# Kernel optimization log

Hardware: AMD Instinct MI355X
Metric: run time of the kernel (lower is better)

Reference implementation:

```python
import jax, jax.numpy as jnp
import numpy as np

MEAN_DEG = 3.8
QS = (2, 4, 8, 16, 32, 64)
POOL_DIM = 100
BP_ITERS = 10


def _bn(x, g, b):
    # BatchNorm1d in training mode: biased batch statistics over the node dim
    m = x.mean(0)
    v = ((x - m) ** 2).mean(0)
    return g * (x - m) * jax.lax.rsqrt(v + 1e-5) + b


def _gcn_sparse(x, src, dst, n, w, b):
    # GCNConv: add self loops, symmetric deg^-1/2 normalization, scatter-add aggregation
    loop = jnp.arange(n, dtype=src.dtype)
    s2 = jnp.concatenate([src, loop])
    d2 = jnp.concatenate([dst, loop])
    deg = jax.ops.segment_sum(jnp.ones(s2.shape[0], x.dtype), d2, num_segments=n)
    dinv = jnp.where(deg > 0, jax.lax.rsqrt(deg), 0.0)
    norm = (dinv[s2] * dinv[d2])[:, None]
    return jax.ops.segment_sum((x @ w)[s2] * norm, d2, num_segments=n) + b


def _gcn_dense(x, adj, w, b):
    # GCN on the dense pooled adjacency (pooled graphs are fully connected)
    n = adj.shape[-1]
    A = adj + jnp.eye(n, dtype=adj.dtype)
    d = A.sum(-1)
    dinv = jnp.where(d > 0, jax.lax.rsqrt(d), 0.0)
    An = dinv[:, :, None] * A * dinv[:, None, :]
    return jnp.einsum('bij,bjd->bid', An, x @ w) + b


def _bp(src, dst, n, q, beta, seed):
    # SBM-style belief propagation: iterate node marginals psi [n,q] for a fixed
    # number of sweeps; coupling exp(beta), global external field ~ mean_degree.
    key = jax.random.fold_in(jax.random.key(42), seed)
    psi0 = jax.nn.softmax(jax.random.normal(key, (n, q), jnp.float32), -1)
    eb = jnp.expm1(beta)

    def step(psi, _):
        msg = jax.ops.segment_sum(jnp.log1p(eb * psi[src]), dst, num_segments=n)
        field = (MEAN_DEG * beta / n) * psi.sum(0)
        return jax.nn.softmax(msg - field, -1), None

    psi, _ = jax.lax.scan(step, psi0, None, length=BP_ITERS)
    return psi


def _forward(x, w11, b11, g11, be11, w12, b12, g12, be12, w13, b13, g13, be13,
             bp_betas, pool_w, pool_b,
             w21, b21, g21, be21, w22, b22, g22, be22, w23, b23, g23, be23,
             fc1_w, fc1_b, fc2_w, fc2_b, edge_index, num_graphs):
    n = x.shape[0]
    B = num_graphs
    N = n // B
    src, dst = edge_index[0], edge_index[1]
    # per-graph dense adjacency (edge_index_to_csr -> todense, duplicates sum)
    adj = jnp.zeros((B, N, N), x.dtype).at[src // N, src % N, dst % N].add(1.0)

    # stage 1: three GCN + BN layers on the raw graph
    x11 = _bn(_gcn_sparse(x, src, dst, n, w11, b11), g11, be11)
    x12 = _bn(_gcn_sparse(x11, src, dst, n, w12, b12), g12, be12)
    x13 = _bn(_gcn_sparse(x12, src, dst, n, w13, b13), g13, be13)
    x1_out = jnp.concatenate([x11, x12, x13], -1).reshape(B, N, -1).max(1)  # [B,90]

    # six belief-propagation runs -> concat assignments [n, 2+4+...+64 = 126]
    s1 = jnp.concatenate([_bp(src, dst, n, q, bp_betas[i], i) for i, q in enumerate(QS)], -1)
    s1 = s1 @ pool_w + pool_b  # [n, 100]

    # dense diff-pool
    s1 = jax.nn.softmax(s1.reshape(B, N, POOL_DIM), -1)
    p1_x = jnp.einsum('bnk,bnd->bkd', s1, x13.reshape(B, N, -1))   # [B,100,30]
    p1_adj = jnp.einsum('bnk,bnm,bml->bkl', s1, adj, s1)           # [B,100,100]

    # stage 2: three dense GCN + BN layers on pooled graphs
    C = 30
    x21 = _bn(_gcn_dense(p1_x, p1_adj, w21, b21).reshape(-1, C), g21, be21)
    x22 = _bn(_gcn_dense(x21.reshape(B, POOL_DIM, C), p1_adj, w22, b22).reshape(-1, C), g22, be22)
    x23 = _bn(_gcn_dense(x22.reshape(B, POOL_DIM, C), p1_adj, w23, b23).reshape(-1, C), g23, be23)
    x2_out = jnp.concatenate([x21, x22, x23], -1).reshape(B, POOL_DIM, -1).max(1)  # [B,90]

    conv_out = jnp.concatenate([x1_out, x2_out], -1)  # [B,180]
    out = jax.nn.relu(conv_out @ fc1_w + fc1_b) @ fc2_w + fc2_b  # dropout p=0 -> identity
    return out, jnp.zeros((1,), x.dtype)


def setup_inputs() -> dict:
    key = jax.random.key(0)
    B, N, EP = 64, 1024, 8192
    ks = jax.random.split(key, 24)
    x = jax.random.normal(ks[0], (B * N, 3), jnp.float32)
    off = (jnp.arange(B, dtype=jnp.int32) * N)[:, None]
    src = (jax.random.randint(ks[1], (B, EP), 0, N, jnp.int32) + off).reshape(-1)
    dst = (jax.random.randint(ks[2], (B, EP), 0, N, jnp.int32) + off).reshape(-1)
    edge_index = jnp.stack([src, dst])

    def lin(k, i, o):
        return jax.random.normal(k, (i, o), jnp.float32) / np.sqrt(i)

    p = {}
    dims1 = [(3, 30), (30, 30), (30, 30)]
    for idx, (i, o) in enumerate(dims1, 1):
        p['w1%d' % idx] = lin(ks[2 + idx], i, o)
        p['b1%d' % idx] = jnp.zeros((o,), jnp.float32)
        p['g1%d' % idx] = jnp.ones((o,), jnp.float32)
        p['be1%d' % idx] = jnp.zeros((o,), jnp.float32)
    for idx in (1, 2, 3):
        p['w2%d' % idx] = lin(ks[8 + idx], 30, 30)
        p['b2%d' % idx] = jnp.zeros((30,), jnp.float32)
        p['g2%d' % idx] = jnp.ones((30,), jnp.float32)
        p['be2%d' % idx] = jnp.zeros((30,), jnp.float32)
    qs = np.array(QS, np.float32)
    p['bp_betas'] = jnp.asarray(np.log(qs / (np.sqrt(MEAN_DEG) - 1.0) + 1.0))
    p['pool_w'] = lin(ks[15], 126, 100); p['pool_b'] = jnp.zeros((100,), jnp.float32)
    p['fc1_w'] = lin(ks[16], 180, 50); p['fc1_b'] = jnp.zeros((50,), jnp.float32)
    p['fc2_w'] = lin(ks[17], 50, 6); p['fc2_b'] = jnp.zeros((6,), jnp.float32)
    return {'x': x, 'edge_index': edge_index, 'num_graphs': B, **p}


def reference(x, edge_index, num_graphs, w11, b11, g11, be11, w12, b12, g12, be12,
              w13, b13, g13, be13, bp_betas, pool_w, pool_b,
              w21, b21, g21, be21, w22, b22, g22, be22, w23, b23, g23, be23,
              fc1_w, fc1_b, fc2_w, fc2_b):
    return _forward(x, w11, b11, g11, be11, w12, b12, g12, be12, w13, b13, g13, be13,
                    bp_betas, pool_w, pool_b,
                    w21, b21, g21, be21, w22, b22, g22, be22, w23, b23, g23, be23,
                    fc1_w, fc1_b, fc2_w, fc2_b, edge_index, num_graphs)
```

## Files before the change

### kernel.cpp

```cpp
#include <hip/hip_runtime.h>
#include <stdint.h>
#include <float.h>


constexpr int NN    = 65536;
constexpr int NEDGE = 524288;
constexpr int NBG   = 64;

__constant__ int cQS[6]   = {2,4,8,16,32,64};

__device__ __forceinline__ void tf2x32(uint32_t k0, uint32_t k1, uint32_t x0, uint32_t x1,
                                       uint32_t& o0, uint32_t& o1){
  uint32_t ks[3] = {k0, k1, k0 ^ k1 ^ 0x1BD11BDAu};
  x0 += ks[0]; x1 += ks[1];
  const int RA[4] = {13,15,26,6}, RB[4] = {17,29,16,24};
  #pragma unroll
  for (int i=0;i<5;i++){
    const int* r = (i&1)? RB : RA;
    #pragma unroll
    for (int j=0;j<4;j++){
      x0 += x1;
      x1 = (x1 << r[j]) | (x1 >> (32 - r[j]));
      x1 ^= x0;
    }
    x0 += ks[(i+1)%3];
    x1 += ks[(i+2)%3] + (uint32_t)(i+1);
  }
  o0 = x0; o1 = x1;
}

__device__ __forceinline__ float erfinv32(float xx){
  #pragma clang fp contract(off)
  float w = -log1pf(-xx*xx);
  float p;
  if (w < 5.0f){
    w = w - 2.5f;
    p = 2.81022636e-08f;
    p = 3.43273939e-07f  + p*w;
    p = -3.5233877e-06f  + p*w;
    p = -4.39150654e-06f + p*w;
    p = 0.00021858087f   + p*w;
    p = -0.00125372503f  + p*w;
    p = -0.00417768164f  + p*w;
    p = 0.246640727f     + p*w;
    p = 1.50140941f      + p*w;
  } else {
    w = sqrtf(w) - 3.0f;
    p = -0.000200214257f;
    p = 0.000100950558f  + p*w;
    p = 0.00134934322f   + p*w;
    p = -0.00367342844f  + p*w;
    p = 0.00573950773f   + p*w;
    p = -0.0076224613f   + p*w;
    p = 0.00943887047f   + p*w;
    p = 1.00167406f      + p*w;
    p = 2.83297682f      + p*w;
  }
  return p*xx;
}

__global__ __launch_bounds__(256) void k_count(const int* __restrict__ src, const int* __restrict__ dst,
                                               int* __restrict__ degi, int* __restrict__ dego){
  int e = blockIdx.x*256 + threadIdx.x;
  if (e >= NEDGE) return;
  atomicAdd(&degi[dst[e]], 1);
  atomicAdd(&dego[src[e]], 1);
}

__global__ __launch_bounds__(256) void k_scan1(const int* __restrict__ deg, int* __restrict__ rp,
                                               int* __restrict__ bsum){
  __shared__ int lds[256];
  int b = blockIdx.x, t = threadIdx.x;
  lds[t] = deg[b*256 + t];
  __syncthreads();
  for (int s=1;s<256;s<<=1){
    int add = (t>=s)? lds[t-s] : 0;
    __syncthreads();
    lds[t] += add;
    __syncthreads();
  }
  rp[b*256 + t + 1] = lds[t];
  if (t==0 && b==0) rp[0] = 0;
  if (t==255) bsum[b] = lds[255];
}

__global__ __launch_bounds__(256) void k_scan2(int* __restrict__ bsum){
  __shared__ int lds[256];
  int t = threadIdx.x;
  lds[t] = bsum[t];
  __syncthreads();
  for (int s=1;s<256;s<<=1){
    int add = (t>=s)? lds[t-s] : 0;
    __syncthreads();
    lds[t] += add;
    __syncthreads();
  }
  bsum[t] = (t==0)? 0 : lds[t-1];
}

__global__ __launch_bounds__(256) void k_scan3(int* __restrict__ rp, const int* __restrict__ bsum){
  int b = blockIdx.x, t = threadIdx.x;
  rp[b*256 + t + 1] += bsum[b];
}

__global__ __launch_bounds__(256) void k_fill(const int* __restrict__ key, const int* __restrict__ rp,
                                              int* __restrict__ cnt, int* __restrict__ colbuf){
  int e = blockIdx.x*256 + threadIdx.x;
  if (e >= NEDGE) return;
  int d = key[e];
  int p = atomicAdd(&cnt[d], 1);
  colbuf[rp[d] + p] = e;
}

__global__ __launch_bounds__(256) void k_sortrow(const int* __restrict__ rp, int* __restrict__ colbuf,
                                                 const int* __restrict__ other){
  int v = blockIdx.x*256 + threadIdx.x;
  if (v >= NN) return;
  int s0 = rp[v], s1 = rp[v+1];
  for (int i=s0+1;i<s1;i++){
    int key = colbuf[i]; int j = i-1;
    while (j>=s0 && colbuf[j]>key){ colbuf[j+1]=colbuf[j]; j--; }
    colbuf[j+1] = key;
  }
  for (int i=s0;i<s1;i++) colbuf[i] = other[colbuf[i]];
}

__global__ __launch_bounds__(256) void k_dinv(const int* __restrict__ degi, float* __restrict__ dinv){
  int v = blockIdx.x*256 + threadIdx.x;
  if (v >= NN) return;
  dinv[v] = 1.0f / sqrtf((float)(degi[v] + 1));
}

template<int CIN>
__global__ __launch_bounds__(256) void k_mm30(const float* __restrict__ x, const float* __restrict__ w,
                                              float* __restrict__ h, int nrow){
  __shared__ float ws[CIN*30];
  int t = threadIdx.x;
  for (int i=t;i<CIN*30;i+=256) ws[i] = w[i];
  __syncthreads();
  int id = blockIdx.x*256 + t;
  if (id >= nrow*30) return;
  int v = id/30, j = id - v*30;
  const float* xr = x + v*CIN;
  float acc = 0.f;
  #pragma unroll
  for (int k=0;k<CIN;k++) acc += xr[k]*ws[k*30+j];
  h[id] = acc;
}

__global__ __launch_bounds__(256) void k_gcn_agg(const float* __restrict__ h, const int* __restrict__ rp,
    const int* __restrict__ col, const float* __restrict__ dinv, const float* __restrict__ bias,
    float* __restrict__ y){
  int b = blockIdx.x;
  int xcd = b & 7, i = b >> 3;
  int gs = i/60, j = i - gs*60;
  int graph = gs*8 + xcd;
  int idwg = j*256 + threadIdx.x;
  int rw = idwg/15, pr = idwg - rw*15;
  int v = graph*1024 + rw;
  float dv = dinv[v];
  float accx = 0.f, accy = 0.f;
  int a = rp[v], e = rp[v+1];
  for (; a+4<=e; a+=4){
    int s0=col[a], s1=col[a+1], s2=col[a+2], s3=col[a+3];
    float d0=dinv[s0], d1=dinv[s1], d2=dinv[s2], d3=dinv[s3];
    float2 h0=*(const float2*)(h+s0*30+2*pr), h1=*(const float2*)(h+s1*30+2*pr);
    float2 h2=*(const float2*)(h+s2*30+2*pr), h3=*(const float2*)(h+s3*30+2*pr);
    accx += h0.x*(d0*dv); accy += h0.y*(d0*dv);
    accx += h1.x*(d1*dv); accy += h1.y*(d1*dv);
    accx += h2.x*(d2*dv); accy += h2.y*(d2*dv);
    accx += h3.x*(d3*dv); accy += h3.y*(d3*dv);
  }
  for (; a<e; ++a){
    int s = col[a];
    float w = dinv[s]*dv;
    float2 hv = *(const float2*)(h+s*30+2*pr);
    accx += hv.x*w; accy += hv.y*w;
  }
  float2 hs = *(const float2*)(h + v*30 + 2*pr);
  float w2 = dv*dv;
  accx += hs.x*w2; accy += hs.y*w2;
  float2 o; o.x = accx + bias[2*pr]; o.y = accy + bias[2*pr+1];
  *(float2*)(y + v*30 + 2*pr) = o;
}

__global__ __launch_bounds__(256) void k_bn_stat(const float* __restrict__ x, int nrow,
    float* __restrict__ partS, float* __restrict__ partQ){
  __shared__ float lds[256*31];
  int b = blockIdx.x, t = threadIdx.x;
  int rows = nrow >> 8;
  float as[30], aq[30];
  #pragma unroll
  for (int f=0;f<30;f++){ as[f]=0.f; aq[f]=0.f; }
  for (int r=t; r<rows; r+=256){
    const float* xr = x + (b*rows + r)*30;
    #pragma unroll
    for (int f=0;f<30;f++){ float v = xr[f]; as[f] += v; aq[f] += v*v; }
  }
  #pragma unroll
  for (int f=0;f<30;f++) lds[t*31+f] = as[f];
  __syncthreads();
  for (int s=128;s>0;s>>=1){
    if (t<s){
      #pragma unroll
      for (int f=0;f<30;f++) lds[t*31+f] += lds[(t+s)*31+f];
    }
    __syncthreads();
  }
  if (t<30) partS[b*30+t] = lds[t];
  __syncthreads();
  #pragma unroll
  for (int f=0;f<30;f++) lds[t*31+f] = aq[f];
  __syncthreads();
  for (int s=128;s>0;s>>=1){
    if (t<s){
      #pragma unroll
      for (int f=0;f<30;f++) lds[t*31+f] += lds[(t+s)*31+f];
    }
    __syncthreads();
  }
  if (t<30) partQ[b*30+t] = lds[t];
}

__global__ void k_bn_red2(const float* __restrict__ partS, const float* __restrict__ partQ,
                          float n, float* __restrict__ mean, float* __restrict__ var){
  int f = threadIdx.x;
  if (f >= 30) return;
  float s = 0.f, q = 0.f;
  for (int b=0;b<256;b++){ s += partS[b*30+f]; q += partQ[b*30+f]; }
  float m = s / n;
  mean[f] = m;
  var[f]  = q / n - m*m;
}

__global__ __launch_bounds__(256) void k_bn_apply(const float* __restrict__ x, const float* __restrict__ mean,
    const float* __restrict__ var, const float* __restrict__ g, const float* __restrict__ be,
    float* __restrict__ out, int nrow){
  int id = blockIdx.x*256 + threadIdx.x;
  if (id >= nrow*30) return;
  int f = id % 30;
  out[id] = g[f]*(x[id]-mean[f]) * (1.0f/sqrtf(var[f]+1e-5f)) + be[f];
}

__device__ __forceinline__ void bp_decode2(int b, int& graph, int& run, int& jj){
  int xcd = b & 7, i = b >> 3;
  int gs = i >> 7, j = i & 127;
  if      (j <   4){ run=0; jj=j;    }
  else if (j <   8){ run=1; jj=j-4;  }
  else if (j <  16){ run=2; jj=j-8;  }
  else if (j <  32){ run=3; jj=j-16; }
  else if (j <  64){ run=4; jj=j-32; }
  else             { run=5; jj=j-64; }
  graph = gs*8 + xcd;
}

template<int TPR>
__device__ __forceinline__ void bfly_max4(float& m0, float& m1, float& m2, float& m3){
  if constexpr (TPR > 1){
    #pragma unroll
    for (int lm = TPR>>1; lm; lm >>= 1){
      float p0=__shfl_xor(m0,lm,64), p1=__shfl_xor(m1,lm,64);
      float p2=__shfl_xor(m2,lm,64), p3=__shfl_xor(m3,lm,64);
      m0=fmaxf(m0,p0); m1=fmaxf(m1,p1); m2=fmaxf(m2,p2); m3=fmaxf(m3,p3);
    }
  }
  { float t0=fmaxf(m0,m2), t1=fmaxf(m1,m3), t2=fmaxf(m2,m0), t3=fmaxf(m3,m1);
    m0=t0; m1=t1; m2=t2; m3=t3; }
  { float t0=fmaxf(m0,m1), t1=fmaxf(m1,m0), t2=fmaxf(m2,m3), t3=fmaxf(m3,m2);
    m0=t0; m1=t1; m2=t2; m3=t3; }
}

template<int TPR>
__device__ __forceinline__ void bfly_sum4(float& s0, float& s1, float& s2, float& s3){
  if constexpr (TPR > 1){
    #pragma unroll
    for (int lm = TPR>>1; lm; lm >>= 1){
      float p0=__shfl_xor(s0,lm,64), p1=__shfl_xor(s1,lm,64);
      float p2=__shfl_xor(s2,lm,64), p3=__shfl_xor(s3,lm,64);
      s0 += p0; s1 += p1; s2 += p2; s3 += p3;
    }
  }
  { float t0=s0+s2, t1=s1+s3, t2=s2+s0, t3=s3+s1;
    s0=t0; s1=t1; s2=t2; s3=t3; }
  { float t0=s0+s1, t1=s1+s0, t2=s2+s3, t3=s3+s2;
    s0=t0; s1=t1; s2=t2; s3=t3; }
}

template<int Q, int CO, int TPR, int L2T>
__device__ __forceinline__ void bp_first_elem2(int graph, int jj, float* __restrict__ psi_pk,
                                               float* __restrict__ lg, float eb,
                                               uint32_t k0, uint32_t k1){
  int idx = jj*256 + (int)threadIdx.x;
  if constexpr (Q == 2){
    int row = graph*1024 + idx;
    float z[2];
    #pragma unroll
    for (int r=0;r<2;r++){
      uint32_t b0,b1;
      tf2x32(k0,k1, 0u, (uint32_t)(row*2 + r), b0,b1);
      uint32_t bits = b0 ^ b1;
      float f = __uint_as_float((bits>>9) | 0x3F800000u) - 1.0f;
      const float lo = __uint_as_float(0xBF7FFFFFu);
      float u = fmaxf(lo, f*2.0f + lo);
      z[r] = __uint_as_float(0x3FB504F3u) * erfinv32(u);
    }
    float m0=fmaxf(z[0],z[1]), m1=fmaxf(z[1],z[0]);
    float e0=expf(z[0]-m0), e1=expf(z[1]-m1);
    float s0=e0+e1, s1=e1+e0;
    float p0=e0/s0, p1=e1/s1;
    ((float2*)(psi_pk + (size_t)NN*CO))[row] = make_float2(p0,p1);
    ((float2*)(lg     + (size_t)NN*CO))[row] = make_float2(log1pf(eb*p0), log1pf(eb*p1));
  } else {
    int rw = idx >> L2T, ct = idx & (TPR-1);
    int row = graph*1024 + rw;
    float z[4];
    #pragma unroll
    for (int r=0;r<4;r++){
      uint32_t b0,b1;
      tf2x32(k0,k1, 0u, (uint32_t)(row*Q + 4*ct + r), b0,b1);
      uint32_t bits = b0 ^ b1;
      float f = __uint_as_float((bits>>9) | 0x3F800000u) - 1.0f;
      const float lo = __uint_as_float(0xBF7FFFFFu);
      float u = fmaxf(lo, f*2.0f + lo);
      z[r] = __uint_as_float(0x3FB504F3u) * erfinv32(u);
    }
    float m0=z[0],m1=z[1],m2=z[2],m3=z[3];
    bfly_max4<TPR>(m0,m1,m2,m3);
    float e0=expf(z[0]-m0), e1=expf(z[1]-m1), e2=expf(z[2]-m2), e3=expf(z[3]-m3);
    float s0=e0,s1=e1,s2=e2,s3=e3;
    bfly_sum4<TPR>(s0,s1,s2,s3);
    float p0=e0/s0, p1=e1/s1, p2=e2/s2, p3=e3/s3;
    ((float4*)(psi_pk + (size_t)NN*CO))[(size_t)row*TPR + ct] = make_float4(p0,p1,p2,p3);
    ((float4*)(lg     + (size_t)NN*CO))[(size_t)row*TPR + ct] =
        make_float4(log1pf(eb*p0), log1pf(eb*p1), log1pf(eb*p2), log1pf(eb*p3));
  }
}

__global__ __launch_bounds__(256) void k_bp_first(float* __restrict__ psi_pk, float* __restrict__ lg,
                                                  const float* __restrict__ betas){
  int graph, run, jj;
  bp_decode2(blockIdx.x, graph, run, jj);
  uint32_t k0, k1;
  tf2x32(0u, 42u, 0u, (uint32_t)run, k0, k1);
  float eb = expm1f(betas[run]);
  switch(run){
    case 0: bp_first_elem2< 2, 0, 1,0>(graph, jj, psi_pk, lg, eb, k0, k1); break;
    case 1: bp_first_elem2< 4, 2, 1,0>(graph, jj, psi_pk, lg, eb, k0, k1); break;
    case 2: bp_first_elem2< 8, 6, 2,1>(graph, jj, psi_pk, lg, eb, k0, k1); break;
    case 3: bp_first_elem2<16,14, 4,2>(graph, jj, psi_pk, lg, eb, k0, k1); break;
    case 4: bp_first_elem2<32,30, 8,3>(graph, jj, psi_pk, lg, eb, k0, k1); break;
    default:bp_first_elem2<64,62,16,4>(graph, jj, psi_pk, lg, eb, k0, k1); break;
  }
}

template<int Q, int CO, int TPR, int L2T>
__device__ __forceinline__ void bp_step_elem2(int graph, int run, int jj,
    const float* __restrict__ lcur, float* __restrict__ nxt, float* __restrict__ lnxt,
    const int* __restrict__ rp, const int* __restrict__ col,
    const float* __restrict__ field, float eb, int fin){
  int idx = jj*256 + (int)threadIdx.x;
  if constexpr (Q == 2){
    int row = graph*1024 + idx;
    const float2* B2 = (const float2*)(lcur + (size_t)NN*CO);
    float a0=0.f, a1=0.f;
    int a = rp[row], b2 = rp[row+1];
    for (; a+4<=b2; a+=4){
      int s0=col[a],s1=col[a+1],s2=col[a+2],s3=col[a+3];
      float2 u0=B2[s0], u1=B2[s1], u2=B2[s2], u3=B2[s3];
      a0+=u0.x; a1+=u0.y;
      a0+=u1.x; a1+=u1.y;
      a0+=u2.x; a1+=u2.y;
      a0+=u3.x; a1+=u3.y;
    }
    for (; a<b2; ++a){ float2 u=B2[col[a]]; a0+=u.x; a1+=u.y; }
    float v0 = a0 - field[run*64 + 0];
    float v1 = a1 - field[run*64 + 1];
    float m0=fmaxf(v0,v1), m1=fmaxf(v1,v0);
    float e0=expf(v0-m0), e1=expf(v1-m1);
    float s0=e0+e1, s1=e1+e0;
    float p0=e0/s0, p1=e1/s1;
    if (fin){
      float* o = nxt + (size_t)row*126 + CO;
      o[0]=p0; o[1]=p1;
    } else {
      ((float2*)(nxt  + (size_t)NN*CO))[row] = make_float2(p0,p1);
      ((float2*)(lnxt + (size_t)NN*CO))[row] = make_float2(log1pf(eb*p0), log1pf(eb*p1));
    }
  } else {
    int rw = idx >> L2T, ct = idx & (TPR-1);
    int row = graph*1024 + rw;
    const float4* B4 = (const float4*)(lcur + (size_t)NN*CO);
    float a0=0.f,a1=0.f,a2=0.f,a3=0.f;
    int a = rp[row], b2 = rp[row+1];
    for (; a+4<=b2; a+=4){
      int s0=col[a],s1=col[a+1],s2=col[a+2],s3=col[a+3];
      float4 u0=B4[(size_t)s0*TPR+ct], u1=B4[(size_t)s1*TPR+ct];
      float4 u2=B4[(size_t)s2*TPR+ct], u3=B4[(size_t)s3*TPR+ct];
      a0+=u0.x; a1+=u0.y; a2+=u0.z; a3+=u0.w;
      a0+=u1.x; a1+=u1.y; a2+=u1.z; a3+=u1.w;
      a0+=u2.x; a1+=u2.y; a2+=u2.z; a3+=u2.w;
      a0+=u3.x; a1+=u3.y; a2+=u3.z; a3+=u3.w;
    }
    for (; a<b2; ++a){
      float4 u = B4[(size_t)col[a]*TPR+ct];
      a0+=u.x; a1+=u.y; a2+=u.z; a3+=u.w;
    }
    const float4 fld = *(const float4*)(field + run*64 + 4*ct);
    float v0 = a0 - fld.x, v1 = a1 - fld.y, v2 = a2 - fld.z, v3 = a3 - fld.w;
    float m0=v0,m1=v1,m2=v2,m3=v3;
    bfly_max4<TPR>(m0,m1,m2,m3);
    float e0=expf(v0-m0), e1=expf(v1-m1), e2=expf(v2-m2), e3=expf(v3-m3);
    float s0=e0,s1=e1,s2=e2,s3=e3;
    bfly_sum4<TPR>(s0,s1,s2,s3);
    float p0=e0/s0, p1=e1/s1, p2=e2/s2, p3=e3/s3;
    if (fin){
      float* o = nxt + (size_t)row*126 + CO + 4*ct;
      o[0]=p0; o[1]=p1; o[2]=p2; o[3]=p3;
    } else {
      ((float4*)(nxt  + (size_t)NN*CO))[(size_t)row*TPR+ct] = make_float4(p0,p1,p2,p3);
      ((float4*)(lnxt + (size_t)NN*CO))[(size_t)row*TPR+ct] =
          make_float4(log1pf(eb*p0), log1pf(eb*p1), log1pf(eb*p2), log1pf(eb*p3));
    }
  }
}

__global__ __launch_bounds__(256) void k_bp_step(
    float* __restrict__ nxt, const float* __restrict__ lcur, float* __restrict__ lnxt,
    const int* __restrict__ rp, const int* __restrict__ col,
    const float* __restrict__ field, const float* __restrict__ betas, int fin){
  int graph, run, jj;
  bp_decode2(blockIdx.x, graph, run, jj);
  float eb = expm1f(betas[run]);
  switch(run){
    case 0: bp_step_elem2< 2, 0, 1,0>(graph, run, jj, lcur, nxt, lnxt, rp, col, field, eb, fin); break;
    case 1: bp_step_elem2< 4, 2, 1,0>(graph, run, jj, lcur, nxt, lnxt, rp, col, field, eb, fin); break;
    case 2: bp_step_elem2< 8, 6, 2,1>(graph, run, jj, lcur, nxt, lnxt, rp, col, field, eb, fin); break;
    case 3: bp_step_elem2<16,14, 4,2>(graph, run, jj, lcur, nxt, lnxt, rp, col, field, eb, fin); break;
    case 4: bp_step_elem2<32,30, 8,3>(graph, run, jj, lcur, nxt, lnxt, rp, col, field, eb, fin); break;
    default:bp_step_elem2<64,62,16,4>(graph, run, jj, lcur, nxt, lnxt, rp, col, field, eb, fin); break;
  }
}

__global__ __launch_bounds__(64) void k_colsum_part(const float* __restrict__ psi_pk, float* __restrict__ part){
  int b = blockIdx.x;
  int xcd = b & 7, i = b >> 3;
  int gs = i/24, rem = i - gs*24;
  int run = rem >> 2, cg = rem & 3;
  int graph = gs*8 + xcd;
  int chunk = graph*4 + cg;
  int q = cQS[run];
  int co = (run==0)?0:(run==1)?2:(run==2)?6:(run==3)?14:(run==4)?30:62;
  int c = threadIdx.x;
  if (c >= q) return;
  float s = 0.f;
  const float* p = psi_pk + (size_t)NN*co + (size_t)chunk*256*q + c;
  #pragma unroll 8
  for (int r=0;r<256;r++) s += p[r*q];
  part[(run*256 + chunk)*64 + c] = s;
}

__global__ void k_field(const float* __restrict__ part, const float* __restrict__ betas,
                        float* __restrict__ field){
  int id = threadIdx.x;
  int run = id >> 6, c = id & 63;
  if (c >= cQS[run]) return;
  float s = 0.f;
  for (int b=0;b<256;b++) s += part[(run*256 + b)*64 + c];
  float beta = betas[run];
  field[id] = s * (3.8f*beta/65536.0f);
}

__global__ __launch_bounds__(512) void k_s1(const float* __restrict__ cat, const float* __restrict__ pw,
                                            const float* __restrict__ pb, float* __restrict__ s1){
  __shared__ float wl[12600];
  int t = threadIdx.x;
  for (int i=t;i<12600;i+=512) wl[i] = pw[i];
  int w = t>>6, tl = t&63;
  bool act = tl < 50;
  float pb0 = act? pb[2*tl]   : 0.f;
  float pb1 = act? pb[2*tl+1] : 0.f;
  __syncthreads();
  #pragma unroll
  for (int p=0;p<2;p++){
    int row0 = blockIdx.x*64 + p*32 + w*4;
    float x0[4], x1[4];
    #pragma unroll
    for (int r=0;r<4;r++){
      if (tl < 63){
        float2 xv = *reinterpret_cast<const float2*>(cat + (size_t)(row0+r)*126 + 2*tl);
        x0[r]=xv.x; x1[r]=xv.y;
      } else { x0[r]=0.f; x1[r]=0.f; }
    }
    float a0[4], a1[4];
    #pragma unroll
    for (int r=0;r<4;r++){ a0[r]=pb0; a1[r]=pb1; }
    #pragma unroll 3
    for (int jj=0;jj<63;jj++){
      float2 wA = *reinterpret_cast<const float2*>(&wl[(2*jj  )*100 + 2*tl]);
      float2 wB = *reinterpret_cast<const float2*>(&wl[(2*jj+1)*100 + 2*tl]);
      #pragma unroll
      for (int r=0;r<4;r++){
        float xa = __int_as_float(__builtin_amdgcn_readlane(__float_as_int(x0[r]), jj));
        float xb = __int_as_float(__builtin_amdgcn_readlane(__float_as_int(x1[r]), jj));
        a0[r] += xa*wA.x;
        a1[r] += xa*wA.y;
        a0[r] += xb*wB.x;
        a1[r] += xb*wB.y;
      }
    }
    #pragma unroll
    for (int r=0;r<4;r++){
      float m = act? fmaxf(a0[r], a1[r]) : -FLT_MAX;
      #pragma unroll
      for (int off=32; off; off>>=1) m = fmaxf(m, __shfl_xor(m, off, 64));
      float e0 = act? expf(a0[r]-m) : 0.f;
      float e1 = act? expf(a1[r]-m) : 0.f;
      float ss = e0+e1;
      #pragma unroll
      for (int off=32; off; off>>=1) ss += __shfl_xor(ss, off, 64);
      if (act){
        float2 o; o.x = e0/ss; o.y = e1/ss;
        *reinterpret_cast<float2*>(s1 + (size_t)(row0+r)*100 + 2*tl) = o;
      }
    }
  }
}

__global__ __launch_bounds__(256) void k_T(const float* __restrict__ s1, const int* __restrict__ rp,
                                           const int* __restrict__ col, float* __restrict__ T){
  int b = blockIdx.x;
  int xcd = b & 7, i = b >> 3;
  int gs = i/100, j = i - gs*100;
  int graph = gs*8 + xcd;
  int idwg = j*256 + threadIdx.x;
  int rw = idwg/25, quad = idwg - rw*25;
  int v = graph*1024 + rw;
  float a0=0.f,a1=0.f,a2=0.f,a3=0.f;
  const float4* S4 = (const float4*)s1;
  int a = rp[v], e = rp[v+1];
  for (; a+4<=e; a+=4){
    int s0=col[a], s1_=col[a+1], s2=col[a+2], s3=col[a+3];
    float4 u0=S4[(size_t)s0*25+quad], u1=S4[(size_t)s1_*25+quad];
    float4 u2=S4[(size_t)s2*25+quad], u3=S4[(size_t)s3*25+quad];
    a0+=u0.x; a1+=u0.y; a2+=u0.z; a3+=u0.w;
    a0+=u1.x; a1+=u1.y; a2+=u1.z; a3+=u1.w;
    a0+=u2.x; a1+=u2.y; a2+=u2.z; a3+=u2.w;
    a0+=u3.x; a1+=u3.y; a2+=u3.z; a3+=u3.w;
  }
  for (; a<e; ++a){
    float4 u = S4[(size_t)col[a]*25+quad];
    a0+=u.x; a1+=u.y; a2+=u.z; a3+=u.w;
  }
  ((float4*)T)[(size_t)v*25 + quad] = make_float4(a0,a1,a2,a3);
}

__global__ __launch_bounds__(512) void k_p1adj_sk(const float* __restrict__ s1, const float* __restrict__ T,
                                                  float* __restrict__ part){
  __shared__ float sS[6400];
  __shared__ float sT[6400];
  int blk = blockIdx.x;
  int b = blk >> 2, qtr = blk & 3;
  int t = threadIdx.x;
  int tk = t/20, tl = t - tk*20;
  bool act = t < 500;
  int k0 = tk*4, l0 = tl*5;
  float acc[4][5];
  #pragma unroll
  for (int i=0;i<4;i++)
    #pragma unroll
    for (int j=0;j<5;j++) acc[i][j] = 0.f;
  const float* s1b = s1 + (size_t)b*102400;
  const float* Tb  = T  + (size_t)b*102400;
  for (int c=qtr*4; c<qtr*4+4; c++){
    for (int i=t;i<6400;i+=512){ sS[i] = s1b[c*6400+i]; sT[i] = Tb[c*6400+i]; }
    __syncthreads();
    if (act){
      #pragma unroll 2
      for (int n=0;n<64;n++){
        const float* sr = &sS[n*100 + k0];
        const float* tr = &sT[n*100 + l0];
        float s0=sr[0], s1v=sr[1], s2=sr[2], s3=sr[3];
        float t0=tr[0], t1=tr[1], t2=tr[2], t3=tr[3], t4=tr[4];
        acc[0][0]+=s0*t0; acc[0][1]+=s0*t1; acc[0][2]+=s0*t2; acc[0][3]+=s0*t3; acc[0][4]+=s0*t4;
        acc[1][0]+=s1v*t0; acc[1][1]+=s1v*t1; acc[1][2]+=s1v*t2; acc[1][3]+=s1v*t3; acc[1][4]+=s1v*t4;
        acc[2][0]+=s2*t0; acc[2][1]+=s2*t1; acc[2][2]+=s2*t2; acc[2][3]+=s2*t3; acc[2][4]+=s2*t4;
        acc[3][0]+=s3*t0; acc[3][1]+=s3*t1; acc[3][2]+=s3*t2; acc[3][3]+=s3*t3; acc[3][4]+=s3*t4;
      }
    }
    __syncthreads();
  }
  if (act){
    float* pp = part + (size_t)qtr*640000 + (size_t)b*10000;
    #pragma unroll
    for (int i=0;i<4;i++){
      float* o = pp + (k0+i)*100 + l0;
      #pragma unroll
      for (int j=0;j<5;j++) o[j] = acc[i][j];
    }
  }
}

__global__ __launch_bounds__(256) void k_p1adj_red(const float* __restrict__ part, float* __restrict__ padj){
  int id = blockIdx.x*256 + threadIdx.x;
  if (id >= NBG*10000) return;
  float s = part[id];
  s += part[640000 + id];
  s += part[1280000 + id];
  s += part[1920000 + id];
  padj[id] = s;
}

__global__ __launch_bounds__(256) void k_p1x_sk(const float* __restrict__ s1, const float* __restrict__ x13,
                                                float* __restrict__ part){
  __shared__ float sS[6400];
  __shared__ float sX[1920];
  int blk = blockIdx.x;
  int b = blk >> 2, qtr = blk & 3;
  int t = threadIdx.x;
  int tk = t/10, tl = t - tk*10;
  bool act = t < 250;
  int k0 = tk*4, d0 = tl*3;
  float acc[4][3];
  #pragma unroll
  for (int i=0;i<4;i++)
    #pragma unroll
    for (int j=0;j<3;j++) acc[i][j] = 0.f;
  const float* s1b = s1 + (size_t)b*102400;
  const float* xb  = x13 + (size_t)b*30720;
  for (int c=qtr*4; c<qtr*4+4; c++){
    for (int i=t;i<6400;i+=256) sS[i] = s1b[c*6400+i];
    for (int i=t;i<1920;i+=256) sX[i] = xb[c*1920+i];
    __syncthreads();
    if (act){
      #pragma unroll 2
      for (int n=0;n<64;n++){
        const float* sr = &sS[n*100 + k0];
        const float* xr = &sX[n*30 + d0];
        float s0=sr[0], s1v=sr[1], s2=sr[2], s3=sr[3];
        float x0=xr[0], x1=xr[1], x2=xr[2];
        acc[0][0]+=s0*x0; acc[0][1]+=s0*x1; acc[0][2]+=s0*x2;
        acc[1][0]+=s1v*x0; acc[1][1]+=s1v*x1; acc[1][2]+=s1v*x2;
        acc[2][0]+=s2*x0; acc[2][1]+=s2*x1; acc[2][2]+=s2*x2;
        acc[3][0]+=s3*x0; acc[3][1]+=s3*x1; acc[3][2]+=s3*x2;
      }
    }
    __syncthreads();
  }
  if (act){
    float* pp = part + (size_t)qtr*192000 + (size_t)b*3000;
    #pragma unroll
    for (int i=0;i<4;i++){
      float* o = pp + (k0+i)*30 + d0;
      #pragma unroll
      for (int j=0;j<3;j++) o[j] = acc[i][j];
    }
  }
}

__global__ __launch_bounds__(256) void k_p1x_red(const float* __restrict__ part, float* __restrict__ px){
  int id = blockIdx.x*256 + threadIdx.x;
  if (id >= NBG*3000) return;
  float s = part[id];
  s += part[192000 + id];
  s += part[384000 + id];
  s += part[576000 + id];
  px[id] = s;
}

__global__ __launch_bounds__(256) void k_dinv2(const float* __restrict__ padj, float* __restrict__ dv){
  int id = blockIdx.x*256 + threadIdx.x;
  if (id >= NBG*100) return;
  const float* r = padj + id*100;
  int k = id % 100;
  float s = 0.f;
  for (int l=0;l<100;l++){
    float v = r[l];
    if (l==k) v += 1.0f;
    s += v;
  }
  dv[id] = 1.0f/sqrtf(s);
}

__global__ __launch_bounds__(256) void k_Ank(const float* __restrict__ padj, const float* __restrict__ dv,
                                             float* __restrict__ An){
  int id = blockIdx.x*256 + threadIdx.x;
  if (id >= NBG*10000) return;
  int b = id/10000;
  int rem = id - b*10000;
  int k = rem/100, l = rem - k*100;
  float a = padj[id] + ((k==l)? 1.0f : 0.0f);
  An[id] = (dv[b*100+k]*a)*dv[b*100+l];
}

__global__ __launch_bounds__(256) void k_y2(const float* __restrict__ An, const float* __restrict__ h,
    const float* __restrict__ bias, float* __restrict__ y){
  int id = blockIdx.x*256 + threadIdx.x;
  if (id >= NBG*100*30) return;
  int d = id % 30;
  int bk = id / 30;
  int b = bk / 100;
  const float* Ar = An + bk*100;
  const float* hb = h + b*100*30;
  float acc = 0.f;
  for (int l=0;l<100;l++) acc += Ar[l]*hb[l*30+d];
  y[id] = acc + bias[d];
}

__global__ __launch_bounds__(256) void k_pool2(const float* __restrict__ A,
    const float* __restrict__ Bv, const float* __restrict__ Cv,
    int rows, float* __restrict__ conv, int coff){
  __shared__ float lds[256*31];
  int b = blockIdx.x, a = blockIdx.y, t = threadIdx.x;
  const float* X = (a==0)? A : ((a==1)? Bv : Cv);
  float acc[30];
  #pragma unroll
  for (int f=0;f<30;f++) acc[f] = -FLT_MAX;
  for (int r=t; r<rows; r+=256){
    const float* xr = X + (size_t)(b*rows + r)*30;
    #pragma unroll
    for (int f=0;f<30;f++) acc[f] = fmaxf(acc[f], xr[f]);
  }
  #pragma unroll
  for (int f=0;f<30;f++) lds[t*31+f] = acc[f];
  __syncthreads();
  for (int s=128;s>0;s>>=1){
    if (t<s){
      #pragma unroll
      for (int f=0;f<30;f++) lds[t*31+f] = fmaxf(lds[t*31+f], lds[(t+s)*31+f]);
    }
    __syncthreads();
  }
  if (t<30) conv[b*180 + coff + a*30 + t] = lds[t];
}

__global__ __launch_bounds__(64) void k_fc(const float* __restrict__ conv,
    const float* __restrict__ w1, const float* __restrict__ b1,
    const float* __restrict__ w2, const float* __restrict__ b2, float* __restrict__ out){
  __shared__ float row[180];
  __shared__ float hid[50];
  int b = blockIdx.x, t = threadIdx.x;
  for (int i=t;i<180;i+=64) row[i] = conv[b*180+i];
  __syncthreads();
  if (t < 50){
    float a = b1[t];
    for (int i=0;i<180;i++) a += row[i]*w1[i*50+t];
    hid[t] = fmaxf(a, 0.f);
  }
  __syncthreads();
  if (t < 6){
    float a = b2[t];
    for (int i=0;i<50;i++) a += hid[i]*w2[i*6+t];
    out[b*6+t] = a;
  }
  if (b==0 && t==63) out[NBG*6] = 0.0f;
}

extern "C" void kernel_launch(void* const* d_in, const int* in_sizes, int n_in,
                              void* d_out, int out_size, void* d_ws, size_t ws_size,
                              hipStream_t stream)
{
  (void)in_sizes; (void)n_in; (void)out_size; (void)ws_size;
  const float* x   = (const float*)d_in[0];
  const int*   src = (const int*)d_in[1];
  const int*   dst = src + NEDGE;
  const float* w11=(const float*)d_in[3],  *b11=(const float*)d_in[4],  *g11=(const float*)d_in[5],  *be11=(const float*)d_in[6];
  const float* w12=(const float*)d_in[7],  *b12=(const float*)d_in[8],  *g12=(const float*)d_in[9],  *be12=(const float*)d_in[10];
  const float* w13=(const float*)d_in[11], *b13=(const float*)d_in[12], *g13=(const float*)d_in[13], *be13=(const float*)d_in[14];
  const float* w21=(const float*)d_in[15], *b21=(const float*)d_in[16], *g21=(const float*)d_in[17], *be21=(const float*)d_in[18];
  const float* w22=(const float*)d_in[19], *b22=(const float*)d_in[20], *g22=(const float*)d_in[21], *be22=(const float*)d_in[22];
  const float* w23=(const float*)d_in[23], *b23=(const float*)d_in[24], *g23=(const float*)d_in[25], *be23=(const float*)d_in[26];
  const float* betas=(const float*)d_in[27];
  const float* poolw=(const float*)d_in[28], *poolb=(const float*)d_in[29];
  const float* fc1w=(const float*)d_in[30], *fc1b=(const float*)d_in[31];
  const float* fc2w=(const float*)d_in[32], *fc2b=(const float*)d_in[33];
  float* out = (float*)d_out;

  uint8_t* basep = (uint8_t*)d_ws;
  size_t off = 0;
  auto take = [&](size_t bytes)->void*{
    void* p = basep + off;
    off = (off + bytes + 255) & ~(size_t)255;
    return p;
  };
  int* degi    = (int*)take((size_t)NN*4);
  int* dego    = (int*)take((size_t)NN*4);
  int* cntA    = (int*)take((size_t)NN*4);
  int* cntB    = (int*)take((size_t)NN*4);
  int* rp_in   = (int*)take((size_t)(NN+1)*4);
  int* rp_out  = (int*)take((size_t)(NN+1)*4);
  int* bsum    = (int*)take(256*4);
  int* col_in  = (int*)take((size_t)NEDGE*4);
  int* col_out = (int*)take((size_t)NEDGE*4);
  float* dinv  = (float*)take((size_t)NN*4);
  float* hbuf  = (float*)take((size_t)NN*30*4);
  float* tmpY  = (float*)take((size_t)NN*30*4);
  float* X1    = (float*)take((size_t)NN*30*4);
  float* X2    = (float*)take((size_t)NN*30*4);
  float* X3    = (float*)take((size_t)NN*30*4);
  float* bufA  = (float*)take((size_t)NN*126*4);
  float* bufB  = (float*)take((size_t)NN*126*4);
  float* logA  = (float*)take((size_t)NN*126*4);
  float* logB  = (float*)take((size_t)NN*126*4);
  float* partCS= (float*)take((size_t)6*256*64*4);
  float* fieldv= (float*)take(384*4);
  float* partBN= (float*)take(256*30*4);
  float* partBN2=(float*)take(256*30*4);
  float* meanv = (float*)take(128);
  float* varv  = (float*)take(128);
  float* px    = (float*)take(192000*4);
  float* padj  = (float*)take(640000*4);
  float* An    = (float*)take(640000*4);
  float* dinv2 = (float*)take(6400*4);
  float* h2    = (float*)take(192000*4);
  float* y2    = (float*)take(192000*4);
  float* X21   = (float*)take(192000*4);
  float* X22   = (float*)take(192000*4);
  float* X23   = (float*)take(192000*4);
  float* conv  = (float*)take(64*180*4);

  float* pAdjPart = logB;
  float* pPxPart  = logB + 2560000;

  hipMemsetAsync(degi, 0, (size_t)NN*4, stream);
  hipMemsetAsync(dego, 0, (size_t)NN*4, stream);
  hipMemsetAsync(cntA, 0, (size_t)NN*4, stream);
  hipMemsetAsync(cntB, 0, (size_t)NN*4, stream);
  k_count<<<2048,256,0,stream>>>(src,dst,degi,dego);
  k_scan1<<<256,256,0,stream>>>(degi, rp_in, bsum);
  k_scan2<<<1,256,0,stream>>>(bsum);
  k_scan3<<<256,256,0,stream>>>(rp_in, bsum);
  k_scan1<<<256,256,0,stream>>>(dego, rp_out, bsum);
  k_scan2<<<1,256,0,stream>>>(bsum);
  k_scan3<<<256,256,0,stream>>>(rp_out, bsum);
  k_fill<<<2048,256,0,stream>>>(dst, rp_in, cntA, col_in);
  k_fill<<<2048,256,0,stream>>>(src, rp_out, cntB, col_out);
  k_sortrow<<<256,256,0,stream>>>(rp_in,  col_in,  src);
  k_sortrow<<<256,256,0,stream>>>(rp_out, col_out, dst);
  k_dinv<<<256,256,0,stream>>>(degi, dinv);

  auto run_bn = [&](const float* yin, float* xout, const float* g, const float* be, int nrow){
    k_bn_stat<<<256,256,0,stream>>>(yin, nrow, partBN, partBN2);
    k_bn_red2<<<1,32,0,stream>>>(partBN, partBN2, (float)nrow, meanv, varv);
    k_bn_apply<<<(nrow*30)/256,256,0,stream>>>(yin, meanv, varv, g, be, xout, nrow);
  };

  k_mm30<3><<<7680,256,0,stream>>>(x, w11, hbuf, NN);
  k_gcn_agg<<<3840,256,0,stream>>>(hbuf, rp_in, col_in, dinv, b11, tmpY);
  run_bn(tmpY, X1, g11, be11, NN);
  k_mm30<30><<<7680,256,0,stream>>>(X1, w12, hbuf, NN);
  k_gcn_agg<<<3840,256,0,stream>>>(hbuf, rp_in, col_in, dinv, b12, tmpY);
  run_bn(tmpY, X2, g12, be12, NN);
  k_mm30<30><<<7680,256,0,stream>>>(X2, w13, hbuf, NN);
  k_gcn_agg<<<3840,256,0,stream>>>(hbuf, rp_in, col_in, dinv, b13, tmpY);
  run_bn(tmpY, X3, g13, be13, NN);
  k_pool2<<<dim3(NBG,3),256,0,stream>>>(X1, X2, X3, 1024, conv, 0);

  k_bp_first<<<8192,256,0,stream>>>(bufA, logA, betas);
  float* cur = bufA;  float* nxt = bufB;
  float* lcur = logA; float* lnxt = logB;
  for (int it=0; it<10; ++it){
    k_colsum_part<<<1536,64,0,stream>>>(cur, partCS);
    k_field<<<1,384,0,stream>>>(partCS, betas, fieldv);
    int fin = (it==9);
    k_bp_step<<<8192,256,0,stream>>>(nxt, lcur, lnxt, rp_in, col_in, fieldv, betas, fin);
    float* tp = cur;  cur = nxt;   nxt = tp;
    float* tl = lcur; lcur = lnxt; lnxt = tl;
  }

  k_s1<<<1024,512,0,stream>>>(bufA, poolw, poolb, bufB);
  k_T<<<6400,256,0,stream>>>(bufB, rp_out, col_out, bufA);
  k_p1adj_sk<<<256,512,0,stream>>>(bufB, bufA, pAdjPart);
  k_p1adj_red<<<2500,256,0,stream>>>(pAdjPart, padj);
  k_p1x_sk<<<256,256,0,stream>>>(bufB, X3, pPxPart);
  k_p1x_red<<<750,256,0,stream>>>(pPxPart, px);
  k_dinv2<<<25,256,0,stream>>>(padj, dinv2);
  k_Ank<<<2500,256,0,stream>>>(padj, dinv2, An);

  auto gcn2 = [&](const float* xin, const float* w, const float* bb, const float* g,
                  const float* be, float* xout){
    k_mm30<30><<<750,256,0,stream>>>(xin, w, h2, NBG*100);
    k_y2<<<750,256,0,stream>>>(An, h2, bb, y2);
    run_bn(y2, xout, g, be, NBG*100);
  };
  gcn2(px,  w21, b21, g21, be21, X21);
  gcn2(X21, w22, b22, g22, be22, X22);
  gcn2(X22, w23, b23, g23, be23, X23);
  k_pool2<<<dim3(NBG,3),256,0,stream>>>(X21, X22, X23, 100, conv, 90);

  k_fc<<<64,64,0,stream>>>(conv, fc1w, fc1b, fc2w, fc2b, out);
}
```

Before: 1.363 ms.

## Merge CSR build launches, unroll gathers, vectorize colsum, transpose-based pool softmax

Merges the paired in/out CSR build kernels (scan, fill, sortrow) into single launches using blockIdx.y, and replaces the four memsets with one, assuming degi, dego, cntA and cntB are contiguous. Adds 8-way unrolled gather loops in the BP step and k_T so more loads are in flight, and vectorizes the column-sum partial with float4 reads for q>=4. Replaces the readlane-based pool projection with a transpose kernel plus a per-thread 50-accumulator matmul and softmax split across two waves. The new pool path adds an extra transpose pass and higher register pressure.

```diff
diff --git a/kernel.cpp b/kernel.cpp
--- a/kernel.cpp
+++ b/kernel.cpp
@@ -67,9 +67,13 @@
   atomicAdd(&dego[src[e]], 1);
 }
 
-__global__ __launch_bounds__(256) void k_scan1(const int* __restrict__ deg, int* __restrict__ rp,
+__global__ __launch_bounds__(256) void k_scan1(const int* __restrict__ degi, const int* __restrict__ dego,
+                                               int* __restrict__ rpi, int* __restrict__ rpo,
                                                int* __restrict__ bsum){
   __shared__ int lds[256];
+  const int* deg = blockIdx.y? dego : degi;
+  int* rp = blockIdx.y? rpo : rpi;
+  int* bs = bsum + blockIdx.y*256;
   int b = blockIdx.x, t = threadIdx.x;
   lds[t] = deg[b*256 + t];
   __syncthreads();
@@ -81,13 +85,14 @@
   }
   rp[b*256 + t + 1] = lds[t];
   if (t==0 && b==0) rp[0] = 0;
-  if (t==255) bsum[b] = lds[255];
+  if (t==255) bs[b] = lds[255];
 }
 
 __global__ __launch_bounds__(256) void k_scan2(int* __restrict__ bsum){
   __shared__ int lds[256];
+  int* bs = bsum + blockIdx.x*256;
   int t = threadIdx.x;
-  lds[t] = bsum[t];
+  lds[t] = bs[t];
   __syncthreads();
   for (int s=1;s<256;s<<=1){
     int add = (t>=s)? lds[t-s] : 0;
@@ -95,25 +100,40 @@
     lds[t] += add;
     __syncthreads();
   }
-  bsum[t] = (t==0)? 0 : lds[t-1];
-}
-
-__global__ __launch_bounds__(256) void k_scan3(int* __restrict__ rp, const int* __restrict__ bsum){
+  bs[t] = (t==0)? 0 : lds[t-1];
+}
+
+__global__ __launch_bounds__(256) void k_scan3(int* __restrict__ rpi, int* __restrict__ rpo,
+                                               const int* __restrict__ bsum){
+  int* rp = blockIdx.y? rpo : rpi;
+  const int* bs = bsum + blockIdx.y*256;
   int b = blockIdx.x, t = threadIdx.x;
-  rp[b*256 + t + 1] += bsum[b];
-}
-
-__global__ __launch_bounds__(256) void k_fill(const int* __restrict__ key, const int* __restrict__ rp,
-                                              int* __restrict__ cnt, int* __restrict__ colbuf){
+  rp[b*256 + t + 1] += bs[b];
+}
+
+__global__ __launch_bounds__(256) void k_fill(const int* __restrict__ src, const int* __restrict__ dst,
+                                              const int* __restrict__ rpi, const int* __restrict__ rpo,
+                                              int* __restrict__ cntA, int* __restrict__ cntB,
+                                              int* __restrict__ colI, int* __restrict__ colO){
   int e = blockIdx.x*256 + threadIdx.x;
   if (e >= NEDGE) return;
-  int d = key[e];
-  int p = atomicAdd(&cnt[d], 1);
-  colbuf[rp[d] + p] = e;
-}
-
-__global__ __launch_bounds__(256) void k_sortrow(const int* __restrict__ rp, int* __restrict__ colbuf,
-                                                 const int* __restrict__ other){
+  if (blockIdx.y == 0){
+    int d = dst[e];
+    int p = atomicAdd(&cntA[d], 1);
+    colI[rpi[d] + p] = e;
+  } else {
+    int d = src[e];
+    int p = atomicAdd(&cntB[d], 1);
+    colO[rpo[d] + p] = e;
+  }
+}
+
+__global__ __launch_bounds__(256) void k_sortrow(const int* __restrict__ rpi, const int* __restrict__ rpo,
+                                                 int* __restrict__ colI, int* __restrict__ colO,
+                                                 const int* __restrict__ src, const int* __restrict__ dst){
+  const int* rp = blockIdx.y? rpo : rpi;
+  int* colbuf   = blockIdx.y? colO : colI;
+  const int* other = blockIdx.y? dst : src;
   int v = blockIdx.x*256 + threadIdx.x;
   if (v >= NN) return;
   int s0 = rp[v], s1 = rp[v+1];
@@ -364,13 +384,21 @@
     const float2* B2 = (const float2*)(lcur + (size_t)NN*CO);
     float a0=0.f, a1=0.f;
     int a = rp[row], b2 = rp[row+1];
+    for (; a+8<=b2; a+=8){
+      int s0=col[a],s1=col[a+1],s2=col[a+2],s3=col[a+3];
+      int s4=col[a+4],s5=col[a+5],s6=col[a+6],s7=col[a+7];
+      float2 u0=B2[s0], u1=B2[s1], u2=B2[s2], u3=B2[s3];
+      float2 u4=B2[s4], u5=B2[s5], u6=B2[s6], u7=B2[s7];
+      a0+=u0.x; a1+=u0.y; a0+=u1.x; a1+=u1.y;
+      a0+=u2.x; a1+=u2.y; a0+=u3.x; a1+=u3.y;
+      a0+=u4.x; a1+=u4.y; a0+=u5.x; a1+=u5.y;
+      a0+=u6.x; a1+=u6.y; a0+=u7.x; a1+=u7.y;
+    }
     for (; a+4<=b2; a+=4){
       int s0=col[a],s1=col[a+1],s2=col[a+2],s3=col[a+3];
       float2 u0=B2[s0], u1=B2[s1], u2=B2[s2], u3=B2[s3];
-      a0+=u0.x; a1+=u0.y;
-      a0+=u1.x; a1+=u1.y;
-      a0+=u2.x; a1+=u2.y;
-      a0+=u3.x; a1+=u3.y;
+      a0+=u0.x; a1+=u0.y; a0+=u1.x; a1+=u1.y;
+      a0+=u2.x; a1+=u2.y; a0+=u3.x; a1+=u3.y;
     }
     for (; a<b2; ++a){ float2 u=B2[col[a]]; a0+=u.x; a1+=u.y; }
     float v0 = a0 - field[run*64 + 0];
@@ -392,6 +420,22 @@
     const float4* B4 = (const float4*)(lcur + (size_t)NN*CO);
     float a0=0.f,a1=0.f,a2=0.f,a3=0.f;
     int a = rp[row], b2 = rp[row+1];
+    for (; a+8<=b2; a+=8){
+      int s0=col[a],s1=col[a+1],s2=col[a+2],s3=col[a+3];
+      int s4=col[a+4],s5=col[a+5],s6=col[a+6],s7=col[a+7];
+      float4 u0=B4[(size_t)s0*TPR+ct], u1=B4[(size_t)s1*TPR+ct];
+      float4 u2=B4[(size_t)s2*TPR+ct], u3=B4[(size_t)s3*TPR+ct];
+      float4 u4=B4[(size_t)s4*TPR+ct], u5=B4[(size_t)s5*TPR+ct];
+      float4 u6=B4[(size_t)s6*TPR+ct], u7=B4[(size_t)s7*TPR+ct];
+      a0+=u0.x; a1+=u0.y; a2+=u0.z; a3+=u0.w;
+      a0+=u1.x; a1+=u1.y; a2+=u1.z; a3+=u1.w;
+      a0+=u2.x; a1+=u2.y; a2+=u2.z; a3+=u2.w;
+      a0+=u3.x; a1+=u3.y; a2+=u3.z; a3+=u3.w;
+      a0+=u4.x; a1+=u4.y; a2+=u4.z; a3+=u4.w;
+      a0+=u5.x; a1+=u5.y; a2+=u5.z; a3+=u5.w;
+      a0+=u6.x; a1+=u6.y; a2+=u6.z; a3+=u6.w;
+      a0+=u7.x; a1+=u7.y; a2+=u7.z; a3+=u7.w;
+    }
     for (; a+4<=b2; a+=4){
       int s0=col[a],s1=col[a+1],s2=col[a+2],s3=col[a+3];
       float4 u0=B4[(size_t)s0*TPR+ct], u1=B4[(size_t)s1*TPR+ct];
@@ -451,12 +495,26 @@
   int q = cQS[run];
   int co = (run==0)?0:(run==1)?2:(run==2)?6:(run==3)?14:(run==4)?30:62;
   int c = threadIdx.x;
-  if (c >= q) return;
-  float s = 0.f;
-  const float* p = psi_pk + (size_t)NN*co + (size_t)chunk*256*q + c;
-  #pragma unroll 8
-  for (int r=0;r<256;r++) s += p[r*q];
-  part[(run*256 + chunk)*64 + c] = s;
+  if (q >= 4){
+    int nq = q >> 2;
+    if (c >= nq) return;
+    const float4* p4 = (const float4*)(psi_pk + (size_t)NN*co + (size_t)chunk*256*q) + c;
+    float s0=0.f,s1=0.f,s2=0.f,s3=0.f;
+    #pragma unroll 8
+    for (int r=0;r<256;r++){
+      float4 u = p4[(size_t)r*nq];
+      s0+=u.x; s1+=u.y; s2+=u.z; s3+=u.w;
+    }
+    float* o = part + (run*256 + chunk)*64 + 4*c;
+    o[0]=s0; o[1]=s1; o[2]=s2; o[3]=s3;
+  } else {
+    if (c >= q) return;
+    float s = 0.f;
+    const float* p = psi_pk + (size_t)NN*co + (size_t)chunk*256*q + c;
+    #pragma unroll 8
+    for (int r=0;r<256;r++) s += p[r*q];
+    part[(run*256 + chunk)*64 + c] = s;
+  }
 }
 
 __global__ void k_field(const float* __restrict__ part, const float* __restrict__ betas,
@@ -470,59 +528,65 @@
   field[id] = s * (3.8f*beta/65536.0f);
 }
 
-__global__ __launch_bounds__(512) void k_s1(const float* __restrict__ cat, const float* __restrict__ pw,
-                                            const float* __restrict__ pb, float* __restrict__ s1){
+__global__ __launch_bounds__(256) void k_catT(const float* __restrict__ cat, float* __restrict__ catT){
+  __shared__ float tile[64*127];
+  int b = blockIdx.x, t = threadIdx.x;
+  const float* src = cat + (size_t)b*64*126;
+  for (int i=t;i<8064;i+=256){
+    int r = i/126, k = i - r*126;
+    tile[r*127 + k] = src[i];
+  }
+  __syncthreads();
+  for (int i=t;i<8064;i+=256){
+    int k = i>>6, r = i&63;
+    catT[(size_t)k*65536 + b*64 + r] = tile[r*127 + k];
+  }
+}
+
+__global__ __launch_bounds__(256) void k_s1t(const float* __restrict__ catT, const float* __restrict__ pw,
+                                             const float* __restrict__ pb, float* __restrict__ s1){
   __shared__ float wl[12600];
+  __shared__ float pbl[100];
+  __shared__ float redM[2][128];
+  __shared__ float redS[2][128];
   int t = threadIdx.x;
-  for (int i=t;i<12600;i+=512) wl[i] = pw[i];
-  int w = t>>6, tl = t&63;
-  bool act = tl < 50;
-  float pb0 = act? pb[2*tl]   : 0.f;
-  float pb1 = act? pb[2*tl+1] : 0.f;
-  __syncthreads();
-  #pragma unroll
-  for (int p=0;p<2;p++){
-    int row0 = blockIdx.x*64 + p*32 + w*4;
-    float x0[4], x1[4];
-    #pragma unroll
-    for (int r=0;r<4;r++){
-      if (tl < 63){
-        float2 xv = *reinterpret_cast<const float2*>(cat + (size_t)(row0+r)*126 + 2*tl);
-        x0[r]=xv.x; x1[r]=xv.y;
-      } else { x0[r]=0.f; x1[r]=0.f; }
-    }
-    float a0[4], a1[4];
-    #pragma unroll
-    for (int r=0;r<4;r++){ a0[r]=pb0; a1[r]=pb1; }
-    #pragma unroll 3
-    for (int jj=0;jj<63;jj++){
-      float2 wA = *reinterpret_cast<const float2*>(&wl[(2*jj  )*100 + 2*tl]);
-      float2 wB = *reinterpret_cast<const float2*>(&wl[(2*jj+1)*100 + 2*tl]);
-      #pragma unroll
-      for (int r=0;r<4;r++){
-        float xa = __int_as_float(__builtin_amdgcn_readlane(__float_as_int(x0[r]), jj));
-        float xb = __int_as_float(__builtin_amdgcn_readlane(__float_as_int(x1[r]), jj));
-        a0[r] += xa*wA.x;
-        a1[r] += xa*wA.y;
-        a0[r] += xb*wB.x;
-        a1[r] += xb*wB.y;
-      }
-    }
-    #pragma unroll
-    for (int r=0;r<4;r++){
-      float m = act? fmaxf(a0[r], a1[r]) : -FLT_MAX;
-      #pragma unroll
-      for (int off=32; off; off>>=1) m = fmaxf(m, __shfl_xor(m, off, 64));
-      float e0 = act? expf(a0[r]-m) : 0.f;
-      float e1 = act? expf(a1[r]-m) : 0.f;
-      float ss = e0+e1;
-      #pragma unroll
-      for (int off=32; off; off>>=1) ss += __shfl_xor(ss, off, 64);
-      if (act){
-        float2 o; o.x = e0/ss; o.y = e1/ss;
-        *reinterpret_cast<float2*>(s1 + (size_t)(row0+r)*100 + 2*tl) = o;
-      }
-    }
+  for (int i=t;i<12600;i+=256) wl[i] = pw[i];
+  if (t < 100) pbl[t] = pb[t];
+  int w = t>>6, lane = t&63;
+  int rh = w&1, chh = w>>1;
+  int ch = chh*50;
+  int row = blockIdx.x*128 + rh*64 + lane;
+  __syncthreads();
+  float acc[50];
+  #pragma unroll
+  for (int j=0;j<50;j++) acc[j] = pbl[ch+j];
+  for (int k=0;k<126;k++){
+    float xv = catT[(size_t)k*65536 + row];
+    const float* wr = &wl[k*100 + ch];
+    #pragma unroll
+    for (int j=0;j<50;j+=2){
+      float2 wv = *(const float2*)&wr[j];
+      acc[j]   += xv*wv.x;
+      acc[j+1] += xv*wv.y;
+    }
+  }
+  float m = acc[0];
+  #pragma unroll
+  for (int j=1;j<50;j++) m = fmaxf(m, acc[j]);
+  redM[chh][rh*64 + lane] = m;
+  __syncthreads();
+  float mm = fmaxf(redM[0][rh*64 + lane], redM[1][rh*64 + lane]);
+  float s = 0.f;
+  #pragma unroll
+  for (int j=0;j<50;j++){ acc[j] = expf(acc[j]-mm); s += acc[j]; }
+  redS[chh][rh*64 + lane] = s;
+  __syncthreads();
+  float tot = redS[0][rh*64 + lane] + redS[1][rh*64 + lane];
+  float* o = s1 + (size_t)row*100 + ch;
+  #pragma unroll
+  for (int j=0;j<50;j+=2){
+    float2 ov; ov.x = acc[j]/tot; ov.y = acc[j+1]/tot;
+    *(float2*)&o[j] = ov;
   }
 }
 
@@ -538,6 +602,22 @@
   float a0=0.f,a1=0.f,a2=0.f,a3=0.f;
   const float4* S4 = (const float4*)s1;
   int a = rp[v], e = rp[v+1];
+  for (; a+8<=e; a+=8){
+    int s0=col[a], s1_=col[a+1], s2=col[a+2], s3=col[a+3];
+    int s4=col[a+4], s5=col[a+5], s6=col[a+6], s7=col[a+7];
+    float4 u0=S4[(size_t)s0*25+quad], u1=S4[(size_t)s1_*25+quad];
+    float4 u2=S4[(size_t)s2*25+quad], u3=S4[(size_t)s3*25+quad];
+    float4 u4=S4[(size_t)s4*25+quad], u5=S4[(size_t)s5*25+quad];
+    float4 u6=S4[(size_t)s6*25+quad], u7=S4[(size_t)s7*25+quad];
+    a0+=u0.x; a1+=u0.y; a2+=u0.z; a3+=u0.w;
+    a0+=u1.x; a1+=u1.y; a2+=u1.z; a3+=u1.w;
+    a0+=u2.x; a1+=u2.y; a2+=u2.z; a3+=u2.w;
+    a0+=u3.x; a1+=u3.y; a2+=u3.z; a3+=u3.w;
+    a0+=u4.x; a1+=u4.y; a2+=u4.z; a3+=u4.w;
+    a0+=u5.x; a1+=u5.y; a2+=u5.z; a3+=u5.w;
+    a0+=u6.x; a1+=u6.y; a2+=u6.z; a3+=u6.w;
+    a0+=u7.x; a1+=u7.y; a2+=u7.z; a3+=u7.w;
+  }
   for (; a+4<=e; a+=4){
     int s0=col[a], s1_=col[a+1], s2=col[a+2], s3=col[a+3];
     float4 u0=S4[(size_t)s0*25+quad], u1=S4[(size_t)s1_*25+quad];
@@ -788,7 +868,7 @@
   int* cntB    = (int*)take((size_t)NN*4);
   int* rp_in   = (int*)take((size_t)(NN+1)*4);
   int* rp_out  = (int*)take((size_t)(NN+1)*4);
-  int* bsum    = (int*)take(256*4);
+  int* bsum    = (int*)take(512*4);
   int* col_in  = (int*)take((size_t)NEDGE*4);
   int* col_out = (int*)take((size_t)NEDGE*4);
   float* dinv  = (float*)take((size_t)NN*4);
@@ -818,24 +898,17 @@
   float* X23   = (float*)take(192000*4);
   float* conv  = (float*)take(64*180*4);
 
+  float* catT     = logA;
   float* pAdjPart = logB;
   float* pPxPart  = logB + 2560000;
 
-  hipMemsetAsync(degi, 0, (size_t)NN*4, stream);
-  hipMemsetAsync(dego, 0, (size_t)NN*4, stream);
-  hipMemsetAsync(cntA, 0, (size_t)NN*4, stream);
-  hipMemsetAsync(cntB, 0, (size_t)NN*4, stream);
+  hipMemsetAsync(degi, 0, (size_t)4*NN*4, stream);
   k_count<<<2048,256,0,stream>>>(src,dst,degi,dego);
-  k_scan1<<<256,256,0,stream>>>(degi, rp_in, bsum);
-  k_scan2<<<1,256,0,stream>>>(bsum);
-  k_scan3<<<256,256,0,stream>>>(rp_in, bsum);
-  k_scan1<<<256,256,0,stream>>>(dego, rp_out, bsum);
-  k_scan2<<<1,256,0,stream>>>(bsum);
-  k_scan3<<<256,256,0,stream>>>(rp_out, bsum);
-  k_fill<<<2048,256,0,stream>>>(dst, rp_in, cntA, col_in);
-  k_fill<<<2048,256,0,stream>>>(src, rp_out, cntB, col_out);
-  k_sortrow<<<256,256,0,stream>>>(rp_in,  col_in,  src);
-  k_sortrow<<<256,256,0,stream>>>(rp_out, col_out, dst);
+  k_scan1<<<dim3(256,2),256,0,stream>>>(degi, dego, rp_in, rp_out, bsum);
+  k_scan2<<<2,256,0,stream>>>(bsum);
+  k_scan3<<<dim3(256,2),256,0,stream>>>(rp_in, rp_out, bsum);
+  k_fill<<<dim3(2048,2),256,0,stream>>>(src, dst, rp_in, rp_out, cntA, cntB, col_in, col_out);
+  k_sortrow<<<dim3(256,2),256,0,stream>>>(rp_in, rp_out, col_in, col_out, src, dst);
   k_dinv<<<256,256,0,stream>>>(degi, dinv);
 
   auto run_bn = [&](const float* yin, float* xout, const float* g, const float* be, int nrow){
@@ -867,7 +940,8 @@
     float* tl = lcur; lcur = lnxt; lnxt = tl;
   }
 
-  k_s1<<<1024,512,0,stream>>>(bufA, poolw, poolb, bufB);
+  k_catT<<<1024,256,0,stream>>>(bufA, catT);
+  k_s1t<<<512,256,0,stream>>>(catT, poolw, poolb, bufB);
   k_T<<<6400,256,0,stream>>>(bufB, rp_out, col_out, bufA);
   k_p1adj_sk<<<256,512,0,stream>>>(bufB, bufA, pAdjPart);
   k_p1adj_red<<<2500,256,0,stream>>>(pAdjPart, padj);
```

After: 1.345 ms. About the same (-1.3%).
